# Kernel optimization log

Hardware: AMD Instinct MI355X
Metric: run time of the kernel (lower is better)

## Reference

```python
import jax, jax.numpy as jnp
import numpy as np

N = 65536          # total nodes
B = 64             # graphs in batch
NPG = N // B       # nodes per graph (equal-size graphs)
K = 128            # n_clusters (assignment dim)
D_IN = 128         # node feature dim
D = 128            # pooled feature dim
E = 1048576        # edges (avg degree 16)


def setup_inputs() -> dict:
    key = jax.random.key(0)
    k1, k2, k3, k4, k5, k6 = jax.random.split(key, 6)
    h = jax.random.normal(k1, (N, D_IN), dtype=jnp.float32)
    fea = jax.random.normal(k2, (B * K, D), dtype=jnp.float32)
    W_self = jax.random.normal(k3, (D_IN, K), dtype=jnp.float32) / np.sqrt(D_IN)
    W_neigh = jax.random.normal(k4, (D_IN, K), dtype=jnp.float32) / np.sqrt(D_IN)
    b = jnp.zeros((K,), dtype=jnp.float32)
    # edges kept within each graph: sample local ids then offset by graph base
    base = jnp.repeat(jnp.arange(B, dtype=jnp.int64) * NPG, E // B)
    edge_src = jax.random.randint(k5, (E,), 0, NPG, dtype=jnp.int64) + base
    edge_dst = jax.random.randint(k6, (E,), 0, NPG, dtype=jnp.int64) + base
    return {"h": h, "fea": fea, "W_self": W_self, "W_neigh": W_neigh,
            "b": b, "edge_src": edge_src, "edge_dst": edge_dst}


def reference(h, fea, W_self, W_neigh, b, edge_src, edge_dst):
    # GraphSage mean aggregation: neigh[i] = mean_{j: (j->i)} h[j]
    deg = jnp.zeros((N,), h.dtype).at[edge_dst].add(1.0)
    neigh = jnp.zeros((N, D_IN), h.dtype).at[edge_dst].add(h[edge_src])
    neigh = neigh / jnp.maximum(deg, 1.0)[:, None]
    assign = jax.nn.relu(h @ W_self + neigh @ W_neigh + b)       # [N, K]
    assign = jax.nn.softmax(assign, axis=1)                       # softmax over clusters
    # block-diagonal mm == per-graph GEMM: [B, n, K] @ [B, K, D] -> [B, n, D]
    out = jnp.einsum('bnk,bkd->bnd',
                     assign.reshape(B, NPG, K),
                     fea.reshape(B, K, D))
    return out.reshape(N, D)
```

## Files before the change

kernel.cpp:

```cpp
#include <hip/hip_runtime.h>

#define N_NODES 65536
#define B_G     64
#define NPG     1024
#define KC      128
#define DIN     128
#define E_EDGES 1048576
#define EPG     16384
#define NSLICE  8
#define SLICE_E (EPG / NSLICE)
#define CSTRIDE (EPG + NPG)

typedef __attribute__((ext_vector_type(8))) short short8;
typedef __attribute__((ext_vector_type(4))) float floatx4;

static __device__ __forceinline__ short f2bf(float x) {
    unsigned u = __float_as_uint(x);
    unsigned r = (u + 0x7FFF + ((u >> 16) & 1)) >> 16;
    return (short)r;
}
static __device__ __forceinline__ unsigned pack2(float a, float b) {
    return (unsigned)(unsigned short)f2bf(a) | ((unsigned)(unsigned short)f2bf(b) << 16);
}

__global__ __launch_bounds__(256) void setup_a(
    const float* __restrict__ Wself, const float* __restrict__ Wneigh,
    const float* __restrict__ fea, const float* __restrict__ h,
    const int* __restrict__ edst,
    short* __restrict__ wt, short* __restrict__ feaT, short* __restrict__ h_bf,
    int* __restrict__ slicecnt)
{
    int bid = blockIdx.x;
    int tid = threadIdx.x;
    if (bid < B_G * NSLICE) {
        __shared__ int cnt[NPG];
        int g = bid >> 3, s = bid & 7;
        int gbase = g << 10;
        for (int i = tid; i < NPG; i += 256) cnt[i] = 0;
        __syncthreads();
        const int* ed = edst + (size_t)g * EPG + s * SLICE_E;
#pragma unroll
        for (int it = 0; it < SLICE_E / 256; it++)
            atomicAdd(&cnt[ed[it * 256 + tid] - gbase], 1);
        __syncthreads();
        int* sc = slicecnt + ((size_t)bid << 10);
        for (int i = tid; i < NPG; i += 256) sc[i] = cnt[i];
    } else {
        long idx = (long)(bid - B_G * NSLICE) * 256 + tid;
        if (idx < 32768) {
            int n = (int)(idx >> 8), k = (int)(idx & 255);
            float v = (k < 128) ? Wself[k * 128 + n] : Wneigh[(k - 128) * 128 + n];
            wt[idx] = f2bf(v);
        } else if (idx < 32768 + 1048576) {
            long fi = idx - 32768;
            int g = (int)(fi >> 14), d = (int)((fi >> 7) & 127), k = (int)(fi & 127);
            feaT[fi] = f2bf(fea[((long)g * 128 + k) * 128 + d]);
        } else {
            long gi = idx - 32768 - 1048576;
            const float4* hp = (const float4*)h + gi * 2;
            float4 a = hp[0], b4 = hp[1];
            uint4 w;
            w.x = pack2(a.x, a.y);
            w.y = pack2(a.z, a.w);
            w.z = pack2(b4.x, b4.y);
            w.w = pack2(b4.z, b4.w);
            ((uint4*)h_bf)[gi] = w;
        }
    }
}

__global__ __launch_bounds__(1024) void setup_b(
    const int* __restrict__ slicecnt, int* __restrict__ offs,
    int* __restrict__ deg, int* __restrict__ sliceoffs)
{
    __shared__ int sa[NPG];
    int g = blockIdx.x;
    int tid = threadIdx.x;
    int s8[NSLICE];
    int d = 0;
#pragma unroll
    for (int s = 0; s < NSLICE; s++) {
        s8[s] = slicecnt[(((size_t)g * NSLICE + s) << 10) + tid];
        d += s8[s];
    }
    int p = (d + 1) & ~1;
    sa[tid] = p;
    __syncthreads();
    for (int off = 1; off < NPG; off <<= 1) {
        int v = sa[tid];
        int vv = (tid >= off) ? sa[tid - off] : 0;
        __syncthreads();
        sa[tid] = v + vv;
        __syncthreads();
    }
    int excl = sa[tid] - p;
    offs[(g << 10) + tid] = excl;
    deg[(g << 10) + tid] = d;
    int run = excl;
#pragma unroll
    for (int s = 0; s < NSLICE; s++) {
        sliceoffs[(((size_t)g * NSLICE + s) << 10) + tid] = run;
        run += s8[s];
    }
}

__global__ __launch_bounds__(256) void setup_c(
    const int* __restrict__ esrc, const int* __restrict__ edst,
    const int* __restrict__ sliceoffs, unsigned short* __restrict__ csr)
{
    __shared__ int cur[NPG];
    int bid = blockIdx.x;
    int tid = threadIdx.x;
    int g = bid >> 3, s = bid & 7;
    int gbase = g << 10;
    const int* so = sliceoffs + ((size_t)bid << 10);
    for (int i = tid; i < NPG; i += 256) cur[i] = so[i];
    __syncthreads();
    const int* ed = edst + (size_t)g * EPG + s * SLICE_E;
    const int* es = esrc + (size_t)g * EPG + s * SLICE_E;
    unsigned short* cg = csr + (size_t)g * CSTRIDE;
#pragma unroll
    for (int it = 0; it < SLICE_E / 256; it++) {
        int e = it * 256 + tid;
        int d = ed[e] - gbase;
        int src = es[e] - gbase;
        int pos = atomicAdd(&cur[d], 1);
        cg[pos] = (unsigned short)src;
    }
}

__global__ __launch_bounds__(256) void agg_kernel(
    const short* __restrict__ h_bf, const unsigned short* __restrict__ csr,
    const int* __restrict__ offs, const int* __restrict__ deg,
    short* __restrict__ neigh)
{
    int g = blockIdx.x >> 8;
    int chunk = blockIdx.x & 255;
    int wave = threadIdx.x >> 6, lane = threadIdx.x & 63;
    int local = chunk * 4 + wave;
    int node = g * NPG + local;
    int start = offs[node];
    int m = deg[node];
    const unsigned short* lst = csr + (size_t)g * CSTRIDE + start;
    const uint2* rows = (const uint2*)h_bf + (size_t)g * NPG * 32;
    int l31 = lane & 31;
    int hi = lane >> 5;
    float s0 = 0.f, s1 = 0.f, s2 = 0.f, s3 = 0.f;
    int pairs = m >> 1;
    int p = 0;
    for (; p + 4 <= pairs; p += 4) {
        unsigned pp[4];
#pragma unroll
        for (int u = 0; u < 4; u++) pp[u] = *(const unsigned*)(lst + 2 * (p + u));
        uint2 v[4];
#pragma unroll
        for (int u = 0; u < 4; u++) {
            int s = hi ? (int)(pp[u] >> 16) : (int)(pp[u] & 0xffff);
            v[u] = rows[s * 32 + l31];
        }
#pragma unroll
        for (int u = 0; u < 4; u++) {
            s0 += __uint_as_float(v[u].x << 16);
            s1 += __uint_as_float(v[u].x & 0xffff0000u);
            s2 += __uint_as_float(v[u].y << 16);
            s3 += __uint_as_float(v[u].y & 0xffff0000u);
        }
    }
    for (; p < pairs; p++) {
        unsigned pp = *(const unsigned*)(lst + 2 * p);
        int s = hi ? (int)(pp >> 16) : (int)(pp & 0xffff);
        uint2 vv = rows[s * 32 + l31];
        s0 += __uint_as_float(vv.x << 16);
        s1 += __uint_as_float(vv.x & 0xffff0000u);
        s2 += __uint_as_float(vv.y << 16);
        s3 += __uint_as_float(vv.y & 0xffff0000u);
    }
    if (m & 1) {
        int s = lst[m - 1];
        if (!hi) {
            uint2 vv = rows[s * 32 + l31];
            s0 += __uint_as_float(vv.x << 16);
            s1 += __uint_as_float(vv.x & 0xffff0000u);
            s2 += __uint_as_float(vv.y << 16);
            s3 += __uint_as_float(vv.y & 0xffff0000u);
        }
    }
    s0 += __shfl_xor(s0, 32, 64);
    s1 += __shfl_xor(s1, 32, 64);
    s2 += __shfl_xor(s2, 32, 64);
    s3 += __shfl_xor(s3, 32, 64);
    if (!hi) {
        float invd = 1.0f / fmaxf((float)m, 1.0f);
        uint2 w;
        w.x = pack2(s0 * invd, s1 * invd);
        w.y = pack2(s2 * invd, s3 * invd);
        ((uint2*)neigh)[(size_t)node * 32 + l31] = w;
    }
}

__global__ __launch_bounds__(256) void fused_kernel(
    const short* __restrict__ h_bf, const short* __restrict__ neigh,
    const short* __restrict__ wt, const float* __restrict__ bias,
    const short* __restrict__ feaT, float* __restrict__ out)
{
    __shared__ __align__(16) short ldsP[128 * 132];

    int tid = threadIdx.x;
    int tile_m = blockIdx.x * 128;
    int g = tile_m >> 10;
    int wave = tid >> 6, lane = tid & 63;
    int l15 = lane & 15, quad = lane >> 4;

    floatx4 zz = {0.f, 0.f, 0.f, 0.f};
    floatx4 acc[2][8];
#pragma unroll
    for (int i = 0; i < 2; i++)
#pragma unroll
        for (int j = 0; j < 8; j++) acc[i][j] = zz;

#pragma unroll
    for (int kk = 0; kk < 4; kk++) {
#pragma unroll
        for (int ks = 0; ks < 2; ks++) {
            int colk = kk * 64 + ks * 32 + quad * 8;
            short8 af[2];
#pragma unroll
            for (int rb = 0; rb < 2; rb++) {
                int m = tile_m + wave * 32 + rb * 16 + l15;
                af[rb] = (kk < 2)
                    ? *reinterpret_cast<const short8*>(h_bf + (size_t)m * DIN + colk)
                    : *reinterpret_cast<const short8*>(neigh + (size_t)m * DIN + (colk - 128));
            }
#pragma unroll
            for (int cb = 0; cb < 8; cb++) {
                int n = cb * 16 + l15;
                short8 bf = *reinterpret_cast<const short8*>(wt + n * 256 + colk);
                acc[0][cb] = __builtin_amdgcn_mfma_f32_16x16x32_bf16(af[0], bf, acc[0][cb], 0, 0, 0);
                acc[1][cb] = __builtin_amdgcn_mfma_f32_16x16x32_bf16(af[1], bf, acc[1][cb], 0, 0, 0);
            }
        }
    }

    float bv[8];
#pragma unroll
    for (int cb = 0; cb < 8; cb++) bv[cb] = bias[cb * 16 + l15];

#pragma unroll
    for (int rb = 0; rb < 2; rb++) {
#pragma unroll
        for (int v = 0; v < 4; v++) {
            float x[8];
            float m = -1e30f;
#pragma unroll
            for (int cb = 0; cb < 8; cb++) {
                float t = acc[rb][cb][v] + bv[cb];
                t = fmaxf(t, 0.f);
                x[cb] = t;
                m = fmaxf(m, t);
            }
#pragma unroll
            for (int off = 1; off < 16; off <<= 1) m = fmaxf(m, __shfl_xor(m, off, 64));
            float s = 0.f;
#pragma unroll
            for (int cb = 0; cb < 8; cb++) { x[cb] = __expf(x[cb] - m); s += x[cb]; }
#pragma unroll
            for (int off = 1; off < 16; off <<= 1) s += __shfl_xor(s, off, 64);
            float inv = 1.0f / s;
            int row = wave * 32 + rb * 16 + quad * 4 + v;
#pragma unroll
            for (int cb = 0; cb < 8; cb++)
                ldsP[row * 132 + cb * 16 + l15] = f2bf(x[cb] * inv);
        }
    }

    asm volatile("s_waitcnt lgkmcnt(0)" ::: "memory");

    floatx4 oacc[2][8];
#pragma unroll
    for (int i = 0; i < 2; i++)
#pragma unroll
        for (int j = 0; j < 8; j++) oacc[i][j] = zz;

    short8 pf[2][4];
#pragma unroll
    for (int rb = 0; rb < 2; rb++)
#pragma unroll
        for (int ks = 0; ks < 4; ks++)
            pf[rb][ks] = *reinterpret_cast<const short8*>(
                ldsP + (wave * 32 + rb * 16 + l15) * 132 + ks * 32 + quad * 8);

#pragma unroll
    for (int cb = 0; cb < 8; cb++) {
#pragma unroll
        for (int ks = 0; ks < 4; ks++) {
            short8 bf = *reinterpret_cast<const short8*>(
                feaT + ((size_t)g * 128 + cb * 16 + l15) * 128 + ks * 32 + quad * 8);
            oacc[0][cb] = __builtin_amdgcn_mfma_f32_16x16x32_bf16(pf[0][ks], bf, oacc[0][cb], 0, 0, 0);
            oacc[1][cb] = __builtin_amdgcn_mfma_f32_16x16x32_bf16(pf[1][ks], bf, oacc[1][cb], 0, 0, 0);
        }
    }

#pragma unroll
    for (int rb = 0; rb < 2; rb++)
#pragma unroll
        for (int v = 0; v < 4; v++) {
            int row = tile_m + wave * 32 + rb * 16 + quad * 4 + v;
#pragma unroll
            for (int cb = 0; cb < 8; cb++)
                out[(size_t)row * 128 + cb * 16 + l15] = oacc[rb][cb][v];
        }
}

extern "C" void kernel_launch(void* const* d_in, const int* in_sizes, int n_in,
                              void* d_out, int out_size, void* d_ws, size_t ws_size,
                              hipStream_t stream) {
    const float* h      = (const float*)d_in[0];
    const float* fea    = (const float*)d_in[1];
    const float* Wself  = (const float*)d_in[2];
    const float* Wneigh = (const float*)d_in[3];
    const float* bias   = (const float*)d_in[4];
    const int*   esrc   = (const int*)d_in[5];
    const int*   edst   = (const int*)d_in[6];
    float* out = (float*)d_out;

    char* ws = (char*)d_ws;
    short* h_bf = (short*)ws;
    size_t off = (size_t)N_NODES * DIN * sizeof(short);
    short* neigh = (short*)(ws + off); off += (size_t)N_NODES * DIN * sizeof(short);
    short* wt    = (short*)(ws + off); off += (size_t)128 * 256 * sizeof(short);
    short* feaT  = (short*)(ws + off); off += (size_t)B_G * 128 * 128 * sizeof(short);
    unsigned short* csr = (unsigned short*)(ws + off); off += (size_t)B_G * CSTRIDE * sizeof(short);
    int* offs = (int*)(ws + off); off += (size_t)N_NODES * sizeof(int);
    int* deg  = (int*)(ws + off); off += (size_t)N_NODES * sizeof(int);
    int* slicecnt  = (int*)(ws + off); off += (size_t)B_G * NSLICE * NPG * sizeof(int);
    int* sliceoffs = (int*)(ws + off);

    setup_a<<<B_G * NSLICE + 8320, 256, 0, stream>>>(Wself, Wneigh, fea, h, edst,
                                                     wt, feaT, h_bf, slicecnt);
    setup_b<<<B_G, 1024, 0, stream>>>(slicecnt, offs, deg, sliceoffs);
    setup_c<<<B_G * NSLICE, 256, 0, stream>>>(esrc, edst, sliceoffs, csr);
    agg_kernel<<<256 * B_G, 256, 0, stream>>>(h_bf, csr, offs, deg, neigh);
    fused_kernel<<<N_NODES / 128, 256, 0, stream>>>(h_bf, neigh, wt, bias, feaT, out);
}
```

Before: 187.9 us.

## Stage weight and fea tiles in LDS for fused assign/pool kernel

The weight matrix is now cooperatively loaded into two padded LDS buffers at kernel start, and the per-graph feaT tile is prefetched into registers during softmax and then written to LDS. Both GEMMs read their B operands from LDS instead of issuing strided global loads from every wave. The change adds extra __syncthreads barriers and doubles LDS use to about 67 KB per block, which may reduce occupancy.

```diff
diff --git a/kernel.cpp b/kernel.cpp
--- a/kernel.cpp
+++ b/kernel.cpp
@@ -203,13 +203,34 @@
     const short* __restrict__ wt, const float* __restrict__ bias,
     const short* __restrict__ feaT, float* __restrict__ out)
 {
-    __shared__ __align__(16) short ldsP[128 * 132];
+    __shared__ __align__(16) short ldsW[128 * 132];
+    __shared__ __align__(16) short ldsY[128 * 132];
 
     int tid = threadIdx.x;
     int tile_m = blockIdx.x * 128;
     int g = tile_m >> 10;
     int wave = tid >> 6, lane = tid & 63;
     int l15 = lane & 15, quad = lane >> 4;
+
+    int wrow = tid >> 1;
+    int wcol = (tid & 1) * 64;
+
+    {
+        const short* s1 = wt + wrow * 256 + wcol;
+        const short* s2 = wt + wrow * 256 + 128 + wcol;
+        short* d1 = ldsW + wrow * 132 + wcol;
+        short* d2 = ldsY + wrow * 132 + wcol;
+        short8 t1[8], t2[8];
+#pragma unroll
+        for (int i = 0; i < 8; i++) t1[i] = *reinterpret_cast<const short8*>(s1 + i * 8);
+#pragma unroll
+        for (int i = 0; i < 8; i++) t2[i] = *reinterpret_cast<const short8*>(s2 + i * 8);
+#pragma unroll
+        for (int i = 0; i < 8; i++) *reinterpret_cast<short8*>(d1 + i * 8) = t1[i];
+#pragma unroll
+        for (int i = 0; i < 8; i++) *reinterpret_cast<short8*>(d2 + i * 8) = t2[i];
+    }
+    __syncthreads();
 
     floatx4 zz = {0.f, 0.f, 0.f, 0.f};
     floatx4 acc[2][8];
@@ -231,14 +252,24 @@
                     ? *reinterpret_cast<const short8*>(h_bf + (size_t)m * DIN + colk)
                     : *reinterpret_cast<const short8*>(neigh + (size_t)m * DIN + (colk - 128));
             }
+            const short* bbase = (kk < 2) ? (ldsW + (colk))
+                                          : (ldsY + (colk - 128));
 #pragma unroll
             for (int cb = 0; cb < 8; cb++) {
                 int n = cb * 16 + l15;
-                short8 bf = *reinterpret_cast<const short8*>(wt + n * 256 + colk);
+                short8 bf = *reinterpret_cast<const short8*>(bbase + n * 132);
                 acc[0][cb] = __builtin_amdgcn_mfma_f32_16x16x32_bf16(af[0], bf, acc[0][cb], 0, 0, 0);
                 acc[1][cb] = __builtin_amdgcn_mfma_f32_16x16x32_bf16(af[1], bf, acc[1][cb], 0, 0, 0);
             }
         }
+    }
+    __syncthreads();
+
+    short8 ft[8];
+    {
+        const short* sf = feaT + ((size_t)g * 128 + wrow) * 128 + wcol;
+#pragma unroll
+        for (int i = 0; i < 8; i++) ft[i] = *reinterpret_cast<const short8*>(sf + i * 8);
     }
 
     float bv[8];
@@ -269,11 +300,16 @@
             int row = wave * 32 + rb * 16 + quad * 4 + v;
 #pragma unroll
             for (int cb = 0; cb < 8; cb++)
-                ldsP[row * 132 + cb * 16 + l15] = f2bf(x[cb] * inv);
-        }
-    }
-
-    asm volatile("s_waitcnt lgkmcnt(0)" ::: "memory");
+                ldsY[row * 132 + cb * 16 + l15] = f2bf(x[cb] * inv);
+        }
+    }
+
+    {
+        short* df = ldsW + wrow * 132 + wcol;
+#pragma unroll
+        for (int i = 0; i < 8; i++) *reinterpret_cast<short8*>(df + i * 8) = ft[i];
+    }
+    __syncthreads();
 
     floatx4 oacc[2][8];
 #pragma unroll
@@ -287,14 +323,14 @@
 #pragma unroll
         for (int ks = 0; ks < 4; ks++)
             pf[rb][ks] = *reinterpret_cast<const short8*>(
-                ldsP + (wave * 32 + rb * 16 + l15) * 132 + ks * 32 + quad * 8);
+                ldsY + (wave * 32 + rb * 16 + l15) * 132 + ks * 32 + quad * 8);
 
 #pragma unroll
     for (int cb = 0; cb < 8; cb++) {
 #pragma unroll
         for (int ks = 0; ks < 4; ks++) {
             short8 bf = *reinterpret_cast<const short8*>(
-                feaT + ((size_t)g * 128 + cb * 16 + l15) * 128 + ks * 32 + quad * 8);
+                ldsW + (cb * 16 + l15) * 132 + ks * 32 + quad * 8);
             oacc[0][cb] = __builtin_amdgcn_mfma_f32_16x16x32_bf16(pf[0][ks], bf, oacc[0][cb], 0, 0, 0);
             oacc[1][cb] = __builtin_amdgcn_mfma_f32_16x16x32_bf16(pf[1][ks], bf, oacc[1][cb], 0, 0, 0);
         }
```

Result: faster. 182.7 us (-2.7%).
